# Optimization experiments

Measured on AMD Instinct MI355X. Metric: run time of the kernel, lower is better.

Reference implementation:

```python
import jax, jax.numpy as jnp
import numpy as np

FEATURE_DIM = 256
NUM_STEPS = 3
NUM_GRAPHS = 2048
ATOMS_PER_GRAPH = 64
TOTAL_ATOMS = NUM_GRAPHS * ATOMS_PER_GRAPH


def setup_inputs() -> dict:
    key = jax.random.key(0)
    k_x, k1, k2, k3, k4 = jax.random.split(key, 5)
    H = FEATURE_DIM
    s = 1.0 / np.sqrt(H)
    x = jax.random.normal(k_x, (TOTAL_ATOMS, H), dtype=jnp.float32)
    batch = jnp.repeat(jnp.arange(NUM_GRAPHS, dtype=jnp.int64), ATOMS_PER_GRAPH)
    sizes = jnp.full((NUM_GRAPHS,), ATOMS_PER_GRAPH, dtype=jnp.int64)
    # LSTM params (PyTorch layout: gates ordered i, f, g, o)
    W_ih = jax.random.uniform(k1, (4 * H, H), jnp.float32, -s, s)
    W_hh = jax.random.uniform(k2, (4 * H, H), jnp.float32, -s, s)
    b_ih = jax.random.uniform(k3, (4 * H,), jnp.float32, -s, s)
    b_hh = jax.random.uniform(k4, (4 * H,), jnp.float32, -s, s)
    return {"x": x, "batch": batch, "sizes": sizes,
            "W_ih": W_ih, "W_hh": W_hh, "b_ih": b_ih, "b_hh": b_hh}


def _lstm_cell(u, hx, cx, W_ih, W_hh, b_ih, b_hh):
    # u: input [B,H]; (hx, cx): hidden/cell [B,H]
    gates = u @ W_ih.T + b_ih + hx @ W_hh.T + b_hh  # [B, 4H]
    i, f, g, o = jnp.split(gates, 4, axis=-1)
    i, f, o = jax.nn.sigmoid(i), jax.nn.sigmoid(f), jax.nn.sigmoid(o)
    c = f * cx + i * jnp.tanh(g)
    h = o * jnp.tanh(c)
    return h, c


def _segment_softmax(scores, seg, num_segments):
    m = jax.ops.segment_max(scores, seg, num_segments=num_segments)
    e = jnp.exp(scores - m[seg])
    s = jax.ops.segment_sum(e, seg, num_segments=num_segments)
    return e / s[seg]


def reference(x, batch, sizes, W_ih, W_hh, b_ih, b_hh):
    B = sizes.shape[0]
    H = x.shape[1]
    seg = batch.astype(jnp.int32)
    h = jnp.zeros((B, H), dtype=x.dtype)
    c = jnp.zeros((B, H), dtype=x.dtype)
    q = h
    r = h
    for _ in range(NUM_STEPS):
        # torch code feeds h both as LSTM input and hidden state
        q, c = _lstm_cell(h, h, c, W_ih, W_hh, b_ih, b_hh)
        scores = jnp.sum(x * q[seg], axis=-1)              # [total_atoms]
        attn = _segment_softmax(scores, seg, B)            # per-graph softmax
        r = jax.ops.segment_sum(x * attn[:, None], seg, num_segments=B)  # [B,H]
        h = r  # torch code overwrites the LSTM hidden with r
    return jnp.concatenate([q, r], axis=-1)  # [B, 2H]
```

## Files before the change

kernel.cpp:

```cpp
#include <hip/hip_runtime.h>
#include <math.h>

#define H 256
#define NB 2048
#define APG 64

typedef __attribute__((ext_vector_type(8))) short short8;
typedef __attribute__((ext_vector_type(4))) float f32x4;

__device__ __forceinline__ unsigned short f2bf(float f) {
    unsigned u = __float_as_uint(f);
    u += 0x7fff + ((u >> 16) & 1);
    return (unsigned short)(u >> 16);
}
__device__ __forceinline__ float bf2f(unsigned short s) {
    return __uint_as_float((unsigned)s << 16);
}
__device__ __forceinline__ float sigm(float v) { return 1.f / (1.f + __expf(-v)); }

__global__ void prep_kernel(const float* __restrict__ W_ih, const float* __restrict__ W_hh,
                            const float* __restrict__ b_ih, const float* __restrict__ b_hh,
                            unsigned short* __restrict__ Wr, float* __restrict__ br) {
    int idx = blockIdx.x * 256 + threadIdx.x;
    int wr_row = idx >> 8, k = idx & 255;
    int hcol = wr_row >> 2, gate = wr_row & 3;
    int src = gate * 65536 + hcol * 256 + k;
    Wr[idx] = f2bf(W_ih[src] + W_hh[src]);
    if (idx < 1024) {
        int hc = idx >> 2, gt = idx & 3;
        br[idx] = b_ih[gt * 256 + hc] + b_hh[gt * 256 + hc];
    }
}

__global__ void lstm0(const float* __restrict__ br, float* __restrict__ q1,
                      float* __restrict__ c1) {
    int hc = threadIdx.x;
    float gi = br[hc * 4 + 0], gg = br[hc * 4 + 2], go = br[hc * 4 + 3];
    float si = sigm(gi), so = sigm(go);
    float cn = si * tanhf(gg);
    c1[hc] = cn;
    q1[hc] = so * tanhf(cn);
}

__global__ __launch_bounds__(256)
void gemm_lstm(const unsigned short* __restrict__ hbf, const unsigned short* __restrict__ Wr,
               const float* __restrict__ br, float* __restrict__ c,
               float* __restrict__ qdst, int qstride) {
    __shared__ unsigned short smem[2][64 * 128];
    unsigned short* As = smem[0];
    unsigned short* Bs = smem[1];
    int t = threadIdx.x;
    int r0 = blockIdx.y * 64;
    int w0 = blockIdx.x * 64;
    int c0h = blockIdx.x * 16;
    int lane = t & 63, w = t >> 6;
    int ln = lane & 15, qd = lane >> 4;
    int m0 = w * 16;
    f32x4 acc[4] = {};
    for (int kc = 0; kc < 2; ++kc) {
        #pragma unroll
        for (int p = 0; p < 4; ++p) {
            int gid = p * 256 + t;
            int row = gid >> 4, g = gid & 15;
            int sg = g ^ (row & 15);
            *(short8*)&As[row * 128 + sg * 8] =
                *(const short8*)&hbf[(r0 + row) * H + kc * 128 + g * 8];
            *(short8*)&Bs[row * 128 + sg * 8] =
                *(const short8*)&Wr[(w0 + row) * H + kc * 128 + g * 8];
        }
        __syncthreads();
        #pragma unroll
        for (int kk = 0; kk < 4; ++kk) {
            int ga = (kk * 4 + qd) ^ ln;
            short8 a = *(short8*)&As[(m0 + ln) * 128 + ga * 8];
            #pragma unroll
            for (int t4 = 0; t4 < 4; ++t4) {
                short8 b = *(short8*)&Bs[(t4 * 16 + ln) * 128 + ga * 8];
                acc[t4] = __builtin_amdgcn_mfma_f32_16x16x32_bf16(a, b, acc[t4], 0, 0, 0);
            }
        }
        __syncthreads();
    }
    float* gl = (float*)smem;
    #pragma unroll
    for (int t4 = 0; t4 < 4; ++t4)
        #pragma unroll
        for (int r = 0; r < 4; ++r)
            gl[(m0 + qd * 4 + r) * 68 + t4 * 16 + ln] = acc[t4][r];
    __syncthreads();
    #pragma unroll
    for (int p = 0; p < 4; ++p) {
        int idx = p * 256 + t;
        int row = idx >> 4, hc = idx & 15;
        float4 g4 = *(float4*)&gl[row * 68 + hc * 4];
        float4 b4 = *(const float4*)&br[(c0h + hc) * 4];
        float gi = g4.x + b4.x, gf = g4.y + b4.y, gg = g4.z + b4.z, go = g4.w + b4.w;
        float si = sigm(gi), sf = sigm(gf), so = sigm(go);
        int cidx = (r0 + row) * H + c0h + hc;
        float cn = sf * c[cidx] + si * tanhf(gg);
        c[cidx] = cn;
        qdst[(r0 + row) * qstride + c0h + hc] = so * tanhf(cn);
    }
}

__global__ __launch_bounds__(256)
void attention1(const float* __restrict__ x, const float* __restrict__ q1,
                unsigned short* __restrict__ hbf, const float* __restrict__ c1,
                float* __restrict__ cdst, unsigned short* __restrict__ xbf) {
    __shared__ float sc[64];
    __shared__ float pl[64];
    __shared__ float rpart[4][256];
    int g = blockIdx.x, t = threadIdx.x;
    int lane = t & 63, w = t >> 6;
    const float* xg = x + (size_t)g * APG * H;
    unsigned short* xbg = xbf + (size_t)g * APG * H;
    float4 xa[16];
    #pragma unroll
    for (int i = 0; i < 16; ++i)
        xa[i] = *(const float4*)&xg[(i * 4 + w) * H + lane * 4];
    float4 q4 = *(const float4*)&q1[lane * 4];
    cdst[g * H + t] = c1[t];
    #pragma unroll
    for (int i = 0; i < 16; ++i) {
        ushort4 u;
        u.x = f2bf(xa[i].x); u.y = f2bf(xa[i].y);
        u.z = f2bf(xa[i].z); u.w = f2bf(xa[i].w);
        *(ushort4*)&xbg[(i * 4 + w) * H + lane * 4] = u;
    }
    #pragma unroll
    for (int i = 0; i < 16; ++i) {
        float p = xa[i].x * q4.x + xa[i].y * q4.y + xa[i].z * q4.z + xa[i].w * q4.w;
        #pragma unroll
        for (int s = 32; s > 0; s >>= 1) p += __shfl_xor(p, s, 64);
        if (lane == 0) sc[i * 4 + w] = p;
    }
    __syncthreads();
    if (t < 64) {
        float s = sc[t], m = s;
        #pragma unroll
        for (int d = 32; d > 0; d >>= 1) m = fmaxf(m, __shfl_xor(m, d, 64));
        float e = __expf(s - m), sum = e;
        #pragma unroll
        for (int d = 32; d > 0; d >>= 1) sum += __shfl_xor(sum, d, 64);
        pl[t] = e / sum;
    }
    __syncthreads();
    float4 r4 = {0.f, 0.f, 0.f, 0.f};
    #pragma unroll
    for (int i = 0; i < 16; ++i) {
        float p = pl[i * 4 + w];
        r4.x += p * xa[i].x; r4.y += p * xa[i].y;
        r4.z += p * xa[i].z; r4.w += p * xa[i].w;
    }
    *(float4*)&rpart[w][lane * 4] = r4;
    __syncthreads();
    float o = rpart[0][t] + rpart[1][t] + rpart[2][t] + rpart[3][t];
    hbf[g * H + t] = f2bf(o);
}

__global__ __launch_bounds__(256)
void attention_bf(const unsigned short* __restrict__ xbf, const float* __restrict__ qsrc,
                  int qstride, unsigned short* __restrict__ hbf,
                  float* __restrict__ rf32, int rstride) {
    __shared__ float sc[64];
    __shared__ float pl[64];
    __shared__ float rpart[4][256];
    int g = blockIdx.x, t = threadIdx.x;
    int lane = t & 63, w = t >> 6;
    const unsigned short* xg = xbf + (size_t)g * APG * H;
    ushort4 xa[16];
    #pragma unroll
    for (int i = 0; i < 16; ++i)
        xa[i] = *(const ushort4*)&xg[(i * 4 + w) * H + lane * 4];
    float4 q4 = *(const float4*)&qsrc[g * qstride + lane * 4];
    #pragma unroll
    for (int i = 0; i < 16; ++i) {
        float p = bf2f(xa[i].x) * q4.x + bf2f(xa[i].y) * q4.y
                + bf2f(xa[i].z) * q4.z + bf2f(xa[i].w) * q4.w;
        #pragma unroll
        for (int s = 32; s > 0; s >>= 1) p += __shfl_xor(p, s, 64);
        if (lane == 0) sc[i * 4 + w] = p;
    }
    __syncthreads();
    if (t < 64) {
        float s = sc[t], m = s;
        #pragma unroll
        for (int d = 32; d > 0; d >>= 1) m = fmaxf(m, __shfl_xor(m, d, 64));
        float e = __expf(s - m), sum = e;
        #pragma unroll
        for (int d = 32; d > 0; d >>= 1) sum += __shfl_xor(sum, d, 64);
        pl[t] = e / sum;
    }
    __syncthreads();
    float4 r4 = {0.f, 0.f, 0.f, 0.f};
    #pragma unroll
    for (int i = 0; i < 16; ++i) {
        float p = pl[i * 4 + w];
        r4.x += p * bf2f(xa[i].x); r4.y += p * bf2f(xa[i].y);
        r4.z += p * bf2f(xa[i].z); r4.w += p * bf2f(xa[i].w);
    }
    *(float4*)&rpart[w][lane * 4] = r4;
    __syncthreads();
    float o = rpart[0][t] + rpart[1][t] + rpart[2][t] + rpart[3][t];
    if (hbf)  hbf[g * H + t] = f2bf(o);
    if (rf32) rf32[g * rstride + t] = o;
}

extern "C" void kernel_launch(void* const* d_in, const int* in_sizes, int n_in,
                              void* d_out, int out_size, void* d_ws, size_t ws_size,
                              hipStream_t stream) {
    const float* x    = (const float*)d_in[0];
    const float* W_ih = (const float*)d_in[3];
    const float* W_hh = (const float*)d_in[4];
    const float* b_ih = (const float*)d_in[5];
    const float* b_hh = (const float*)d_in[6];
    float* out = (float*)d_out;

    char* ws = (char*)d_ws;
    unsigned short* Wr   = (unsigned short*)ws;
    float*          br   = (float*)(ws + 524288);
    unsigned short* hbf  = (unsigned short*)(ws + 528384);
    float*          cbuf = (float*)(ws + 1576960);
    float*          qbuf = (float*)(ws + 3674112);
    float*          q1   = (float*)(ws + 5771264);
    float*          c1   = (float*)(ws + 5772288);
    unsigned short* xbf  = (unsigned short*)(ws + 8388608);

    prep_kernel<<<1024, 256, 0, stream>>>(W_ih, W_hh, b_ih, b_hh, Wr, br);
    lstm0<<<1, 256, 0, stream>>>(br, q1, c1);
    attention1<<<2048, 256, 0, stream>>>(x, q1, hbf, c1, cbuf, xbf);
    gemm_lstm<<<dim3(16, 32), 256, 0, stream>>>(hbf, Wr, br, cbuf, qbuf, 256);
    attention_bf<<<2048, 256, 0, stream>>>(xbf, qbuf, 256, hbf, nullptr, 0);
    gemm_lstm<<<dim3(16, 32), 256, 0, stream>>>(hbf, Wr, br, cbuf, out, 512);
    attention_bf<<<2048, 256, 0, stream>>>(xbf, out, 512, nullptr, out + 256, 512);
}
```

Baseline: 264.7 us.

## Fold weight prep and step-0 LSTM into attention1; 8-wide attention layout

The separate weight-prep and step-0 LSTM kernels are removed. attention1 now also converts and packs the combined weights and biases, and computes q for step 0 from the biases on every block. The first gemm_lstm recomputes the initial cell state from the biases instead of reading a materialised cbuf, which also drops a 2 MB write. The attention kernels now give each half-wave one atom, so each lane holds 8 contiguous features with 16-byte loads and the shuffle reduction is shorter. The trade-off is redundant bias math in every block and a reduction layout with more partial sums.

```diff
diff --git a/kernel.cpp b/kernel.cpp
--- a/kernel.cpp
+++ b/kernel.cpp
@@ -2,7 +2,6 @@
 #include <math.h>
 
 #define H 256
-#define NB 2048
 #define APG 64
 
 typedef __attribute__((ext_vector_type(8))) short short8;
@@ -18,34 +17,10 @@
 }
 __device__ __forceinline__ float sigm(float v) { return 1.f / (1.f + __expf(-v)); }
 
-__global__ void prep_kernel(const float* __restrict__ W_ih, const float* __restrict__ W_hh,
-                            const float* __restrict__ b_ih, const float* __restrict__ b_hh,
-                            unsigned short* __restrict__ Wr, float* __restrict__ br) {
-    int idx = blockIdx.x * 256 + threadIdx.x;
-    int wr_row = idx >> 8, k = idx & 255;
-    int hcol = wr_row >> 2, gate = wr_row & 3;
-    int src = gate * 65536 + hcol * 256 + k;
-    Wr[idx] = f2bf(W_ih[src] + W_hh[src]);
-    if (idx < 1024) {
-        int hc = idx >> 2, gt = idx & 3;
-        br[idx] = b_ih[gt * 256 + hc] + b_hh[gt * 256 + hc];
-    }
-}
-
-__global__ void lstm0(const float* __restrict__ br, float* __restrict__ q1,
-                      float* __restrict__ c1) {
-    int hc = threadIdx.x;
-    float gi = br[hc * 4 + 0], gg = br[hc * 4 + 2], go = br[hc * 4 + 3];
-    float si = sigm(gi), so = sigm(go);
-    float cn = si * tanhf(gg);
-    c1[hc] = cn;
-    q1[hc] = so * tanhf(cn);
-}
-
 __global__ __launch_bounds__(256)
 void gemm_lstm(const unsigned short* __restrict__ hbf, const unsigned short* __restrict__ Wr,
                const float* __restrict__ br, float* __restrict__ c,
-               float* __restrict__ qdst, int qstride) {
+               float* __restrict__ qdst, int qstride, int first) {
     __shared__ unsigned short smem[2][64 * 128];
     unsigned short* As = smem[0];
     unsigned short* Bs = smem[1];
@@ -97,42 +72,68 @@
         float gi = g4.x + b4.x, gf = g4.y + b4.y, gg = g4.z + b4.z, go = g4.w + b4.w;
         float si = sigm(gi), sf = sigm(gf), so = sigm(go);
         int cidx = (r0 + row) * H + c0h + hc;
-        float cn = sf * c[cidx] + si * tanhf(gg);
+        float cprev = first ? (sigm(b4.x) * tanhf(b4.z)) : c[cidx];
+        float cn = sf * cprev + si * tanhf(gg);
         c[cidx] = cn;
         qdst[(r0 + row) * qstride + c0h + hc] = so * tanhf(cn);
     }
 }
 
 __global__ __launch_bounds__(256)
-void attention1(const float* __restrict__ x, const float* __restrict__ q1,
-                unsigned short* __restrict__ hbf, const float* __restrict__ c1,
-                float* __restrict__ cdst, unsigned short* __restrict__ xbf) {
+void attention1(const float* __restrict__ x, const float* __restrict__ W_ih,
+                const float* __restrict__ W_hh, const float* __restrict__ b_ih,
+                const float* __restrict__ b_hh, unsigned short* __restrict__ Wr,
+                float* __restrict__ br, unsigned short* __restrict__ hbf,
+                unsigned short* __restrict__ xbf) {
     __shared__ float sc[64];
     __shared__ float pl[64];
-    __shared__ float rpart[4][256];
+    __shared__ float rsm[32 * 66];
     int g = blockIdx.x, t = threadIdx.x;
-    int lane = t & 63, w = t >> 6;
+    int lane = t & 63, w = t >> 6, ln5 = lane & 31, hw = lane >> 5;
+    int j0 = ln5 * 8;
+
+    if (t < 128) {
+        int idx = g * 128 + t;
+        int wr_row = idx >> 8, k = idx & 255;
+        int hcol = wr_row >> 2, gate = wr_row & 3;
+        int src = gate * 65536 + hcol * 256 + k;
+        Wr[idx] = f2bf(W_ih[src] + W_hh[src]);
+        if (g < 8) {
+            int bidx = g * 128 + t;
+            int hc = bidx >> 2, gt = bidx & 3;
+            br[bidx] = b_ih[gt * 256 + hc] + b_hh[gt * 256 + hc];
+        }
+    }
+
+    float q8[8];
+    #pragma unroll
+    for (int j = 0; j < 8; ++j) {
+        float bi = b_ih[j0 + j]       + b_hh[j0 + j];
+        float bg = b_ih[512 + j0 + j] + b_hh[512 + j0 + j];
+        float bo = b_ih[768 + j0 + j] + b_hh[768 + j0 + j];
+        q8[j] = sigm(bo) * tanhf(sigm(bi) * tanhf(bg));
+    }
+
     const float* xg = x + (size_t)g * APG * H;
     unsigned short* xbg = xbf + (size_t)g * APG * H;
-    float4 xa[16];
-    #pragma unroll
-    for (int i = 0; i < 16; ++i)
-        xa[i] = *(const float4*)&xg[(i * 4 + w) * H + lane * 4];
-    float4 q4 = *(const float4*)&q1[lane * 4];
-    cdst[g * H + t] = c1[t];
-    #pragma unroll
-    for (int i = 0; i < 16; ++i) {
-        ushort4 u;
-        u.x = f2bf(xa[i].x); u.y = f2bf(xa[i].y);
-        u.z = f2bf(xa[i].z); u.w = f2bf(xa[i].w);
-        *(ushort4*)&xbg[(i * 4 + w) * H + lane * 4] = u;
-    }
-    #pragma unroll
-    for (int i = 0; i < 16; ++i) {
-        float p = xa[i].x * q4.x + xa[i].y * q4.y + xa[i].z * q4.z + xa[i].w * q4.w;
-        #pragma unroll
-        for (int s = 32; s > 0; s >>= 1) p += __shfl_xor(p, s, 64);
-        if (lane == 0) sc[i * 4 + w] = p;
+    float xa[8][8];
+    #pragma unroll
+    for (int i = 0; i < 8; ++i) {
+        int atom = i * 8 + w * 2 + hw;
+        float4 a = *(const float4*)&xg[atom * H + j0];
+        float4 b = *(const float4*)&xg[atom * H + j0 + 4];
+        xa[i][0] = a.x; xa[i][1] = a.y; xa[i][2] = a.z; xa[i][3] = a.w;
+        xa[i][4] = b.x; xa[i][5] = b.y; xa[i][6] = b.z; xa[i][7] = b.w;
+        short8 u;
+        #pragma unroll
+        for (int j = 0; j < 8; ++j) u[j] = (short)f2bf(xa[i][j]);
+        *(short8*)&xbg[atom * H + j0] = u;
+        float p = 0.f;
+        #pragma unroll
+        for (int j = 0; j < 8; ++j) p += xa[i][j] * q8[j];
+        #pragma unroll
+        for (int s = 16; s > 0; s >>= 1) p += __shfl_xor(p, s, 64);
+        if (ln5 == 0) sc[atom] = p;
     }
     __syncthreads();
     if (t < 64) {
@@ -145,16 +146,20 @@
         pl[t] = e / sum;
     }
     __syncthreads();
-    float4 r4 = {0.f, 0.f, 0.f, 0.f};
-    #pragma unroll
-    for (int i = 0; i < 16; ++i) {
-        float p = pl[i * 4 + w];
-        r4.x += p * xa[i].x; r4.y += p * xa[i].y;
-        r4.z += p * xa[i].z; r4.w += p * xa[i].w;
-    }
-    *(float4*)&rpart[w][lane * 4] = r4;
-    __syncthreads();
-    float o = rpart[0][t] + rpart[1][t] + rpart[2][t] + rpart[3][t];
+    float r8[8] = {};
+    #pragma unroll
+    for (int i = 0; i < 8; ++i) {
+        float p = pl[i * 8 + w * 2 + hw];
+        #pragma unroll
+        for (int j = 0; j < 8; ++j) r8[j] += p * xa[i][j];
+    }
+    int part = w * 2 + hw;
+    *(float4*)&rsm[ln5 * 66 + part * 8]     = make_float4(r8[0], r8[1], r8[2], r8[3]);
+    *(float4*)&rsm[ln5 * 66 + part * 8 + 4] = make_float4(r8[4], r8[5], r8[6], r8[7]);
+    __syncthreads();
+    float o = 0.f;
+    #pragma unroll
+    for (int p = 0; p < 8; ++p) o += rsm[(t >> 3) * 66 + p * 8 + (t & 7)];
     hbf[g * H + t] = f2bf(o);
 }
 
@@ -164,22 +169,27 @@
                   float* __restrict__ rf32, int rstride) {
     __shared__ float sc[64];
     __shared__ float pl[64];
-    __shared__ float rpart[4][256];
+    __shared__ float rsm[32 * 66];
     int g = blockIdx.x, t = threadIdx.x;
-    int lane = t & 63, w = t >> 6;
+    int lane = t & 63, w = t >> 6, ln5 = lane & 31, hw = lane >> 5;
+    int j0 = ln5 * 8;
     const unsigned short* xg = xbf + (size_t)g * APG * H;
-    ushort4 xa[16];
-    #pragma unroll
-    for (int i = 0; i < 16; ++i)
-        xa[i] = *(const ushort4*)&xg[(i * 4 + w) * H + lane * 4];
-    float4 q4 = *(const float4*)&qsrc[g * qstride + lane * 4];
-    #pragma unroll
-    for (int i = 0; i < 16; ++i) {
-        float p = bf2f(xa[i].x) * q4.x + bf2f(xa[i].y) * q4.y
-                + bf2f(xa[i].z) * q4.z + bf2f(xa[i].w) * q4.w;
-        #pragma unroll
-        for (int s = 32; s > 0; s >>= 1) p += __shfl_xor(p, s, 64);
-        if (lane == 0) sc[i * 4 + w] = p;
+    float4 qa = *(const float4*)&qsrc[g * qstride + j0];
+    float4 qb = *(const float4*)&qsrc[g * qstride + j0 + 4];
+    float q8[8] = {qa.x, qa.y, qa.z, qa.w, qb.x, qb.y, qb.z, qb.w};
+    float xa[8][8];
+    #pragma unroll
+    for (int i = 0; i < 8; ++i) {
+        int atom = i * 8 + w * 2 + hw;
+        short8 u = *(const short8*)&xg[atom * H + j0];
+        #pragma unroll
+        for (int j = 0; j < 8; ++j) xa[i][j] = bf2f((unsigned short)u[j]);
+        float p = 0.f;
+        #pragma unroll
+        for (int j = 0; j < 8; ++j) p += xa[i][j] * q8[j];
+        #pragma unroll
+        for (int s = 16; s > 0; s >>= 1) p += __shfl_xor(p, s, 64);
+        if (ln5 == 0) sc[atom] = p;
     }
     __syncthreads();
     if (t < 64) {
@@ -192,16 +202,20 @@
         pl[t] = e / sum;
     }
     __syncthreads();
-    float4 r4 = {0.f, 0.f, 0.f, 0.f};
-    #pragma unroll
-    for (int i = 0; i < 16; ++i) {
-        float p = pl[i * 4 + w];
-        r4.x += p * bf2f(xa[i].x); r4.y += p * bf2f(xa[i].y);
-        r4.z += p * bf2f(xa[i].z); r4.w += p * bf2f(xa[i].w);
-    }
-    *(float4*)&rpart[w][lane * 4] = r4;
-    __syncthreads();
-    float o = rpart[0][t] + rpart[1][t] + rpart[2][t] + rpart[3][t];
+    float r8[8] = {};
+    #pragma unroll
+    for (int i = 0; i < 8; ++i) {
+        float p = pl[i * 8 + w * 2 + hw];
+        #pragma unroll
+        for (int j = 0; j < 8; ++j) r8[j] += p * xa[i][j];
+    }
+    int part = w * 2 + hw;
+    *(float4*)&rsm[ln5 * 66 + part * 8]     = make_float4(r8[0], r8[1], r8[2], r8[3]);
+    *(float4*)&rsm[ln5 * 66 + part * 8 + 4] = make_float4(r8[4], r8[5], r8[6], r8[7]);
+    __syncthreads();
+    float o = 0.f;
+    #pragma unroll
+    for (int p = 0; p < 8; ++p) o += rsm[(t >> 3) * 66 + p * 8 + (t & 7)];
     if (hbf)  hbf[g * H + t] = f2bf(o);
     if (rf32) rf32[g * rstride + t] = o;
 }
@@ -222,15 +236,11 @@
     unsigned short* hbf  = (unsigned short*)(ws + 528384);
     float*          cbuf = (float*)(ws + 1576960);
     float*          qbuf = (float*)(ws + 3674112);
-    float*          q1   = (float*)(ws + 5771264);
-    float*          c1   = (float*)(ws + 5772288);
     unsigned short* xbf  = (unsigned short*)(ws + 8388608);
 
-    prep_kernel<<<1024, 256, 0, stream>>>(W_ih, W_hh, b_ih, b_hh, Wr, br);
-    lstm0<<<1, 256, 0, stream>>>(br, q1, c1);
-    attention1<<<2048, 256, 0, stream>>>(x, q1, hbf, c1, cbuf, xbf);
-    gemm_lstm<<<dim3(16, 32), 256, 0, stream>>>(hbf, Wr, br, cbuf, qbuf, 256);
+    attention1<<<2048, 256, 0, stream>>>(x, W_ih, W_hh, b_ih, b_hh, Wr, br, hbf, xbf);
+    gemm_lstm<<<dim3(16, 32), 256, 0, stream>>>(hbf, Wr, br, cbuf, qbuf, 256, 1);
     attention_bf<<<2048, 256, 0, stream>>>(xbf, qbuf, 256, hbf, nullptr, 0);
-    gemm_lstm<<<dim3(16, 32), 256, 0, stream>>>(hbf, Wr, br, cbuf, out, 512);
+    gemm_lstm<<<dim3(16, 32), 256, 0, stream>>>(hbf, Wr, br, cbuf, out, 512, 0);
     attention_bf<<<2048, 256, 0, stream>>>(xbf, out, 512, nullptr, out + 256, 512);
 }
```

New measurement: 275.7 us. +4.2%, slower.
